# Kernel optimization log

Hardware: AMD Instinct MI355X
Metric: run time of the kernel (lower is better)

The kernel has to match this reference:

```python
import jax, jax.numpy as jnp
import numpy as np

AREA = 4
NUM_HEADS = 4


def _conv1x1(x, w, s, t):
    # 1x1 Conv (bias=False) + folded BatchNorm: per-out-channel scale s, shift t
    y = jnp.einsum('bchw,oc->bohw', x, w)
    return y * s[None, :, None, None] + t[None, :, None, None]


def setup_inputs() -> dict:
    key = jax.random.key(0)
    ks = jax.random.split(key, 9)
    C, heads = 128, NUM_HEADS
    x = jax.random.normal(ks[0], (2, C, 80, 80), jnp.float32)

    def wmat(k, o, i):
        return jax.random.normal(k, (o, i), jnp.float32) * (i ** -0.5)

    def bn(k, n):
        k1, k2 = jax.random.split(k)
        s = 1.0 + 0.05 * jax.random.normal(k1, (n,), jnp.float32)
        t = 0.05 * jax.random.normal(k2, (n,), jnp.float32)
        return s, t

    w_qk = wmat(ks[1], 2 * C, C); s_qk, t_qk = bn(ks[2], 2 * C)
    w_in = wmat(ks[3], C, C); s_in, t_in = bn(ks[4], C)
    w_out = wmat(ks[5], C, C); s_out, t_out = bn(ks[6], C)
    w_fg = jax.random.normal(ks[7], (heads, heads, 1, 5), jnp.float32) * ((5 * heads) ** -0.5)
    s_fg, t_fg = bn(ks[8], heads)
    return dict(x=x, w_qk=w_qk, s_qk=s_qk, t_qk=t_qk, w_in=w_in, s_in=s_in,
                t_in=t_in, w_out=w_out, s_out=s_out, t_out=t_out,
                w_fg=w_fg, s_fg=s_fg, t_fg=t_fg)


def reference(x, w_qk, s_qk, t_qk, w_in, s_in, t_in, w_out, s_out, t_out, w_fg, s_fg, t_fg):
    B, C, H, W = x.shape
    N = H * W
    heads = NUM_HEADS
    hd = C // heads
    inp = x
    # qk projection -> [B, N, 2C]
    qk = _conv1x1(x, w_qk, s_qk, t_qk).reshape(B, 2 * C, N).transpose(0, 2, 1)
    # input-gated values -> [B, N, C]
    v = jax.nn.sigmoid(_conv1x1(x, w_in, s_in, t_in)) * x
    v = v.reshape(B, C, N).transpose(0, 2, 1)
    # area split
    Be, Na = B * AREA, N // AREA
    qk = qk.reshape(Be, Na, 2 * C)
    v = v.reshape(Be, Na, C)
    q, k = qk[..., :C], qk[..., C:]
    q = q.transpose(0, 2, 1).reshape(Be, heads, hd, Na)
    k = k.transpose(0, 2, 1).reshape(Be, heads, hd, Na)
    v = v.transpose(0, 2, 1).reshape(Be, heads, hd, Na)
    # full NxN attention per area/head
    attn = jnp.einsum('bhdn,bhdm->bhnm', q, k) * (hd ** -0.5)
    attn = jax.nn.softmax(attn, axis=-1)
    # forget gate: (1,5) conv mixing heads along last axis, pad (0,2), BN fold, SiLU
    attn = jax.lax.conv_general_dilated(attn, w_fg, (1, 1), ((0, 0), (2, 2)),
                                        dimension_numbers=('NCHW', 'OIHW', 'NCHW'))
    attn = attn * s_fg[None, :, None, None] + t_fg[None, :, None, None]
    attn = jax.nn.silu(attn)
    # v @ attn^T -> [Be, heads, hd, Na]
    o = jnp.einsum('bhdj,bhij->bhdi', v, attn)
    # merge areas back: [Be,Na,h,hd] -> [B,N,C] -> [B,C,H,W]
    o = o.transpose(0, 3, 1, 2).reshape(B, N, C)
    o = o.reshape(B, H, W, C).transpose(0, 3, 1, 2)
    return jax.nn.sigmoid(_conv1x1(o, w_out, s_out, t_out)) * o + inp
```

## Files before the change

kernel.cpp:

```cpp
#include <hip/hip_runtime.h>
#include <hip/hip_bf16.h>
#include <cstdint>

#define CC 128
#define NN 6400
#define NAa 1600
#define HEADS 4
#define HD 32
#define NB 32
#define MT 64

#define P_ROW 68
#define P_HEAD 1096
#define A_ROW 76
#define A_HEAD 1224
#define PW (HEADS * P_HEAD)
#define AW (HEADS * A_HEAD)
#define HB_IDX(par, qs, hh, lo) (((((par)*2 + (qs))*4 + (hh))*16 + (lo)) * 4)
#define XROW 136

typedef __attribute__((ext_vector_type(8))) short bfrag8;
typedef __attribute__((ext_vector_type(4))) float ffrag4;
typedef union { uint2 u2[2]; bfrag8 f8; } cvt16;

#define LOG2E 1.4426950408889634f
#define QSCL (0.17677669529663687f * 1.4426950408889634f)

__device__ __forceinline__ float sigmoid_fast(float y) {
  return __builtin_amdgcn_rcpf(1.0f + __builtin_amdgcn_exp2f(-LOG2E * y));
}
__device__ __forceinline__ unsigned short f2bf(float f) {
  unsigned u = __float_as_uint(f);
  return (unsigned short)((u + 0x7FFFu + ((u >> 16) & 1u)) >> 16);
}
__device__ __forceinline__ unsigned pk2(float a, float b) {
  float2 f2; f2.x = a; f2.y = b;
  __hip_bfloat162 h = __float22bfloat162_rn(f2);
  union { __hip_bfloat162 h2; unsigned u; } cv; cv.h2 = h;
  return cv.u;
}
__device__ __forceinline__ float bfl(unsigned u) { return __uint_as_float(u << 16); }
__device__ __forceinline__ float bfh(unsigned u) { return __uint_as_float(u & 0xFFFF0000u); }

__global__ __launch_bounds__(256) void prep_kernel(
    const float* __restrict__ w_qk, const float* __restrict__ s_qk,
    const float* __restrict__ w_in, const float* __restrict__ s_in,
    const float* __restrict__ w_out, const float* __restrict__ s_out,
    unsigned short* __restrict__ wqkb, unsigned short* __restrict__ wob) {
  const int blk = blockIdx.x, tid = threadIdx.x;
  if (blk < 8) {
    const int r0 = blk * 48;
    for (int i = tid; i < 6144; i += 256) {
      int r = r0 + (i >> 7), c = i & 127;
      float wv, sv;
      if (r < 2 * CC) { wv = w_qk[r * CC + c]; sv = s_qk[r] * (r < CC ? QSCL : 1.0f); }
      else           { wv = w_in[(r - 2 * CC) * CC + c]; sv = s_in[r - 2 * CC]; }
      wqkb[r * CC + c] = f2bf(wv * sv);
    }
  } else {
    const int r0 = (blk - 8) * 64;
    for (int i = tid; i < 8192; i += 256) {
      int r = r0 + (i >> 7), c = i & 127;
      wob[r * CC + c] = f2bf(w_out[r * CC + c] * s_out[r]);
    }
  }
}

__global__ __launch_bounds__(256) void qkv_kernel(
    const float* __restrict__ x, const unsigned short* __restrict__ wqkb,
    const float* __restrict__ t_qk, const float* __restrict__ t_in,
    unsigned short* __restrict__ qt, unsigned short* __restrict__ kt,
    unsigned short* __restrict__ vb) {
  __shared__ __align__(16) unsigned short xb[16 * XROW];
  const int tid = threadIdx.x;
  const int w = tid >> 6, lane = tid & 63, lo = lane & 15, g = lane >> 4;
  const int blk = blockIdx.x;
  const int b = blk / 400, pt = blk - b * 400;
  const int ng0 = pt * 16;
  const int a = ng0 / NAa, na0 = ng0 - a * NAa;
  const int be = b * 4 + a;
  {
    const int c = tid >> 1, half = tid & 1;
    const float* xr = &x[((size_t)(b * CC + c)) * NN + ng0 + 8 * half];
    const float4 f0 = *(const float4*)xr;
    const float4 f1 = *(const float4*)(xr + 4);
    unsigned short* dst = &xb[(8 * half) * XROW + c];
    dst[0 * XROW] = f2bf(f0.x); dst[1 * XROW] = f2bf(f0.y);
    dst[2 * XROW] = f2bf(f0.z); dst[3 * XROW] = f2bf(f0.w);
    dst[4 * XROW] = f2bf(f1.x); dst[5 * XROW] = f2bf(f1.y);
    dst[6 * XROW] = f2bf(f1.z); dst[7 * XROW] = f2bf(f1.w);
  }
  __syncthreads();
  bfrag8 bf[4];
#pragma unroll
  for (int kk = 0; kk < 4; kk++) bf[kk] = *(const bfrag8*)&xb[lo * XROW + kk * 32 + g * 8];
#pragma unroll
  for (int mt6 = 0; mt6 < 6; mt6++) {
    const int rowbase = (w * 6 + mt6) * 16;
    ffrag4 d = {0.f, 0.f, 0.f, 0.f};
#pragma unroll
    for (int kk = 0; kk < 4; kk++) {
      bfrag8 af = *(const bfrag8*)&wqkb[(size_t)(rowbase + lo) * CC + kk * 32 + g * 8];
      d = __builtin_amdgcn_mfma_f32_16x16x32_bf16(af, bf[kk], d, 0, 0, 0);
    }
    const int r0c = rowbase + 4 * g;
    if (r0c < CC) {
      const int h = r0c >> 5, d0 = r0c & 31;
      uint2 pk;
      pk.x = pk2(d[0] + t_qk[r0c] * QSCL, d[1] + t_qk[r0c + 1] * QSCL);
      pk.y = pk2(d[2] + t_qk[r0c + 2] * QSCL, d[3] + t_qk[r0c + 3] * QSCL);
      *(uint2*)&qt[((size_t)(be * HEADS + h) * NAa + na0 + lo) * HD + d0] = pk;
    } else if (r0c < 2 * CC) {
      const int ch = r0c - CC, h = ch >> 5, d0 = ch & 31;
      uint2 pk;
      pk.x = pk2(d[0] + t_qk[r0c], d[1] + t_qk[r0c + 1]);
      pk.y = pk2(d[2] + t_qk[r0c + 2], d[3] + t_qk[r0c + 3]);
      *(uint2*)&kt[((size_t)(be * HEADS + h) * NAa + na0 + lo) * HD + d0] = pk;
    } else {
      const int ch0 = r0c - 2 * CC;
      const uint2 xv = *(const uint2*)&xb[lo * XROW + ch0];
      float xr[4] = {bfl(xv.x), bfh(xv.x), bfl(xv.y), bfh(xv.y)};
#pragma unroll
      for (int r = 0; r < 4; r++) {
        float y = d[r] + t_in[ch0 + r];
        vb[((size_t)be * CC + ch0 + r) * NAa + na0 + lo] = f2bf(sigmoid_fast(y) * xr[r]);
      }
    }
  }
}

__global__ __launch_bounds__(256) void stats_kernel(
    const unsigned short* __restrict__ qt, const unsigned short* __restrict__ kt,
    float* __restrict__ pstats) {
  int tid = threadIdx.x;
  int h = tid >> 6, lane = tid & 63, lo = lane & 15, g = lane >> 4;
  int bid = blockIdx.x;
  int be = bid & 7;
  int rest = bid >> 3;
  int n0 = (rest % 50) * 32;
  int split = rest / 50;
  int ts0 = split ? 12 : 0, ts1 = split ? 25 : 12;

  const unsigned short* qtb = qt + (size_t)(be * HEADS + h) * NAa * HD;
  const unsigned short* ktb = kt + (size_t)(be * HEADS + h) * NAa * HD;

  bfrag8 qf0 = *(const bfrag8*)(qtb + (size_t)(n0 + lo) * HD + g * 8);
  bfrag8 qf1 = *(const bfrag8*)(qtb + (size_t)(n0 + 16 + lo) * HD + g * 8);
  float sm0[4] = {0.f, 0.f, 0.f, 0.f};
  float sm1[4] = {0.f, 0.f, 0.f, 0.f};
  for (int t = ts0; t < ts1; t++) {
    int m0 = t * MT;
#pragma unroll
    for (int sb = 0; sb < 4; sb++) {
      bfrag8 kf = *(const bfrag8*)(ktb + (size_t)(m0 + sb * 16 + lo) * HD + g * 8);
      ffrag4 z = {0.f, 0.f, 0.f, 0.f};
      ffrag4 c0 = __builtin_amdgcn_mfma_f32_16x16x32_bf16(qf0, kf, z, 0, 0, 0);
      ffrag4 c1 = __builtin_amdgcn_mfma_f32_16x16x32_bf16(qf1, kf, z, 0, 0, 0);
#pragma unroll
      for (int r = 0; r < 4; r++) {
        sm0[r] += __builtin_amdgcn_exp2f(c0[r]);
        sm1[r] += __builtin_amdgcn_exp2f(c1[r]);
      }
    }
  }
#pragma unroll
  for (int r = 0; r < 4; r++) {
#pragma unroll
    for (int off = 1; off <= 8; off <<= 1) {
      sm0[r] += __shfl_xor(sm0[r], off);
      sm1[r] += __shfl_xor(sm1[r], off);
    }
  }
  if (lo == 0) {
    float4 s4; s4.x = sm0[0]; s4.y = sm0[1]; s4.z = sm0[2]; s4.w = sm0[3];
    *(float4*)&pstats[((size_t)(split * 8 + be) * HEADS + h) * NAa + n0 + 4 * g] = s4;
    float4 s5; s5.x = sm1[0]; s5.y = sm1[1]; s5.z = sm1[2]; s5.w = sm1[3];
    *(float4*)&pstats[((size_t)(split * 8 + be) * HEADS + h) * NAa + n0 + 16 + 4 * g] = s5;
  }
}

__global__ __launch_bounds__(512) void apply_kernel(
    const unsigned short* __restrict__ qt, const unsigned short* __restrict__ kt,
    const unsigned short* __restrict__ vb, const float* __restrict__ pstats,
    const float* __restrict__ w_fg, const float* __restrict__ s_fg,
    const float* __restrict__ t_fg, unsigned short* __restrict__ o_part) {
  __shared__ __align__(16) unsigned short Ps[2 * PW];
  __shared__ __align__(16) unsigned short A2s[2 * AW];
  __shared__ __align__(16) unsigned short Hb[1024];
  const int tid = threadIdx.x;
  const int w = tid >> 6, lane = tid & 63, lo = lane & 15, g = lane >> 4;
  const int h = w >> 1, u = w & 1;
  const int bid = blockIdx.x;
  const int be = bid & 7;
  const int rest = bid >> 3;
  const int n0 = (rest % 50) * NB;
  const int split = rest / 50;
  const int ts0 = (split == 0) ? 0 : (split == 1 ? 9 : 17);
  const int tend = (split == 0) ? 9 : (split == 1 ? 17 : 26);
  const int p0 = ts0 & 1;

  const unsigned short* qtb = qt + (size_t)(be * HEADS + h) * NAa * HD;
  const unsigned short* ktb = kt + (size_t)(be * HEADS + h) * NAa * HD;
  const unsigned short* vhb = vb + (size_t)(be * CC + h * HD) * NAa;

  bfrag8 qf[2];
#pragma unroll
  for (int qs = 0; qs < 2; ++qs)
    qf[qs] = *(const bfrag8*)(qtb + (size_t)(n0 + 16 * qs + lo) * HD + g * 8);

  bfrag8 wfrag;
  {
    const int ho = lo >> 2, s = lo & 3;
#pragma unroll
    for (int j = 0; j < 8; j++) {
      const int tp = j - s;
      float wv = (tp >= 0 && tp < 5) ? w_fg[(ho * HEADS + g) * 5 + tp] : 0.0f;
      wfrag[j] = (short)f2bf(wv);
    }
  }
  const float sfv = s_fg[g], tfv = t_fg[g];

  float linv[2];
#pragma unroll
  for (int qs = 0; qs < 2; ++qs) {
    const float den = pstats[((size_t)(0 + be) * HEADS + h) * NAa + n0 + 16 * qs + lo] +
                      pstats[((size_t)(8 + be) * HEADS + h) * NAa + n0 + 16 * qs + lo];
    linv[qs] = -__log2f(den);
  }

  ffrag4 oacc[2][2];
#pragma unroll
  for (int qs = 0; qs < 2; ++qs) {
    ffrag4 z = {0.f, 0.f, 0.f, 0.f};
    oacc[qs][0] = z; oacc[qs][1] = z;
  }

  if (split == 0) {
    if (u == 0 && g == 0) {
      uint2 zz; zz.x = 0; zz.y = 0;
#pragma unroll
      for (int qs = 0; qs < 2; ++qs)
        *(uint2*)&Hb[HB_IDX(p0, qs, h, lo)] = zz;
    }
  } else if (u == 0) {
    bfrag8 kf = *(const bfrag8*)(ktb + (size_t)(ts0 * MT - 16 + lo) * HD + g * 8);
#pragma unroll
    for (int qs = 0; qs < 2; ++qs) {
      ffrag4 cin = {linv[qs], linv[qs], linv[qs], linv[qs]};
      ffrag4 c = __builtin_amdgcn_mfma_f32_16x16x32_bf16(kf, qf[qs], cin, 0, 0, 0);
      if (g == 3) {
        uint2 pk;
        pk.x = pk2(__builtin_amdgcn_exp2f(c[0]), __builtin_amdgcn_exp2f(c[1]));
        pk.y = pk2(__builtin_amdgcn_exp2f(c[2]), __builtin_amdgcn_exp2f(c[3]));
        *(uint2*)&Hb[HB_IDX(p0, qs, h, lo)] = pk;
      }
    }
  }
  {
    const int m0 = ts0 * MT;
#pragma unroll
    for (int sbi = 0; sbi < 2; sbi++) {
      const int sb = 2 * u + sbi;
      bfrag8 kf = *(const bfrag8*)(ktb + (size_t)(m0 + sb * 16 + lo) * HD + g * 8);
#pragma unroll
      for (int qs = 0; qs < 2; ++qs) {
        ffrag4 cin = {linv[qs], linv[qs], linv[qs], linv[qs]};
        ffrag4 c = __builtin_amdgcn_mfma_f32_16x16x32_bf16(kf, qf[qs], cin, 0, 0, 0);
        uint2 pk;
        pk.x = pk2(__builtin_amdgcn_exp2f(c[0]), __builtin_amdgcn_exp2f(c[1]));
        pk.y = pk2(__builtin_amdgcn_exp2f(c[2]), __builtin_amdgcn_exp2f(c[3]));
        *(uint2*)&Ps[qs * PW + h * P_HEAD + lo * P_ROW + 16 * sb + 4 * g] = pk;
        if (sb == 3 && g == 3)
          *(uint2*)&Hb[HB_IDX(p0 ^ 1, qs, h, lo)] = pk;
      }
    }
  }
  __syncthreads();

  for (int t = ts0; t < tend; t++) {
    const int m0 = t * MT;
    const int par = t & 1;
    const bfrag8 vf0 = *(const bfrag8*)(vhb + (size_t)lo * NAa + (m0 - 2 + 32 * u + 8 * g));
    const bfrag8 vf1 = *(const bfrag8*)(vhb + (size_t)(16 + lo) * NAa + (m0 - 2 + 32 * u + 8 * g));
    const bool doqk = (t + 1 < tend);
    const bool realqk = doqk && (t + 1 < 25);
    bfrag8 kf0, kf1;
    if (realqk) {
      const int m1 = (t + 1) * MT;
      kf0 = *(const bfrag8*)(ktb + (size_t)(m1 + (2 * u) * 16 + lo) * HD + g * 8);
      kf1 = *(const bfrag8*)(ktb + (size_t)(m1 + (2 * u + 1) * 16 + lo) * HD + g * 8);
    }
    const bool edge = (t == 0) || (t == 25);
#pragma unroll
    for (int qs = 0; qs < 2; ++qs) {
#pragma unroll
      for (int ii = 0; ii < 2; ii++) {
        const int i = 2 * w + ii;
        cvt16 bb;
        if (i == 0)
          bb.u2[0] = *(const uint2*)&Hb[HB_IDX(par, qs, g, lo)];
        else
          bb.u2[0] = *(const uint2*)&Ps[qs * PW + g * P_HEAD + lo * P_ROW + 4 * i - 4];
        bb.u2[1] = *(const uint2*)&Ps[qs * PW + g * P_HEAD + lo * P_ROW + 4 * i];
        ffrag4 z = {0.f, 0.f, 0.f, 0.f};
        ffrag4 d = __builtin_amdgcn_mfma_f32_16x16x32_bf16(wfrag, bb.f8, z, 0, 0, 0);
        float a2v[4];
        if (edge) {
#pragma unroll
          for (int r = 0; r < 4; r++) {
            const int mp = m0 - 2 + 4 * i + r;
            float y = d[r] * sfv + tfv;
            float v = y * sigmoid_fast(y);
            a2v[r] = (mp >= 0 && mp < NAa) ? v : 0.0f;
          }
        } else {
#pragma unroll
          for (int r = 0; r < 4; r++) {
            float y = d[r] * sfv + tfv;
            a2v[r] = y * sigmoid_fast(y);
          }
        }
        uint2 pk;
        pk.x = pk2(a2v[0], a2v[1]);
        pk.y = pk2(a2v[2], a2v[3]);
        *(uint2*)&A2s[qs * AW + g * A_HEAD + lo * A_ROW + 4 * i] = pk;
      }
    }
    __syncthreads();
    if (doqk) {
      if (realqk) {
#pragma unroll
        for (int qs = 0; qs < 2; ++qs) {
          ffrag4 cin = {linv[qs], linv[qs], linv[qs], linv[qs]};
          ffrag4 c0 = __builtin_amdgcn_mfma_f32_16x16x32_bf16(kf0, qf[qs], cin, 0, 0, 0);
          ffrag4 c1 = __builtin_amdgcn_mfma_f32_16x16x32_bf16(kf1, qf[qs], cin, 0, 0, 0);
          uint2 pk;
          pk.x = pk2(__builtin_amdgcn_exp2f(c0[0]), __builtin_amdgcn_exp2f(c0[1]));
          pk.y = pk2(__builtin_amdgcn_exp2f(c0[2]), __builtin_amdgcn_exp2f(c0[3]));
          *(uint2*)&Ps[qs * PW + h * P_HEAD + lo * P_ROW + 16 * (2 * u) + 4 * g] = pk;
          uint2 pk1;
          pk1.x = pk2(__builtin_amdgcn_exp2f(c1[0]), __builtin_amdgcn_exp2f(c1[1]));
          pk1.y = pk2(__builtin_amdgcn_exp2f(c1[2]), __builtin_amdgcn_exp2f(c1[3]));
          *(uint2*)&Ps[qs * PW + h * P_HEAD + lo * P_ROW + 16 * (2 * u + 1) + 4 * g] = pk1;
          if (u == 1 && g == 3)
            *(uint2*)&Hb[HB_IDX(par, qs, h, lo)] = pk1;
        }
      } else {
        uint2 zz; zz.x = 0; zz.y = 0;
#pragma unroll
        for (int qs = 0; qs < 2; ++qs) {
          *(uint2*)&Ps[qs * PW + h * P_HEAD + lo * P_ROW + 16 * (2 * u) + 4 * g] = zz;
          *(uint2*)&Ps[qs * PW + h * P_HEAD + lo * P_ROW + 16 * (2 * u + 1) + 4 * g] = zz;
        }
      }
    }
#pragma unroll
    for (int qs = 0; qs < 2; ++qs) {
      cvt16 av;
      av.u2[0] = *(const uint2*)&A2s[qs * AW + h * A_HEAD + lo * A_ROW + 32 * u + 8 * g];
      av.u2[1] = *(const uint2*)&A2s[qs * AW + h * A_HEAD + lo * A_ROW + 32 * u + 8 * g + 4];
      oacc[qs][0] = __builtin_amdgcn_mfma_f32_16x16x32_bf16(av.f8, vf0, oacc[qs][0], 0, 0, 0);
      oacc[qs][1] = __builtin_amdgcn_mfma_f32_16x16x32_bf16(av.f8, vf1, oacc[qs][1], 0, 0, 0);
    }
    __syncthreads();
  }

  float* scr = (float*)A2s;
  if (u == 1) {
#pragma unroll
    for (int qs = 0; qs < 2; ++qs) {
      float4 f0; f0.x = oacc[qs][0][0]; f0.y = oacc[qs][0][1]; f0.z = oacc[qs][0][2]; f0.w = oacc[qs][0][3];
      float4 f1; f1.x = oacc[qs][1][0]; f1.y = oacc[qs][1][1]; f1.z = oacc[qs][1][2]; f1.w = oacc[qs][1][3];
      *(float4*)&scr[((qs * 4 + h) * 64 + lane) * 8] = f0;
      *(float4*)&scr[((qs * 4 + h) * 64 + lane) * 8 + 4] = f1;
    }
  }
  __syncthreads();
  if (u == 0) {
#pragma unroll
    for (int qs = 0; qs < 2; ++qs) {
      const float4 f0 = *(const float4*)&scr[((qs * 4 + h) * 64 + lane) * 8];
      const float4 f1 = *(const float4*)&scr[((qs * 4 + h) * 64 + lane) * 8 + 4];
      const float fa[4] = {f0.x, f0.y, f0.z, f0.w};
      const float fb[4] = {f1.x, f1.y, f1.z, f1.w};
#pragma unroll
      for (int r = 0; r < 4; r++) {
        const size_t rowoff = ((size_t)(split * 8 + be) * NAa + n0 + 16 * qs + 4 * g + r) * CC;
        o_part[rowoff + h * HD + lo] = f2bf(oacc[qs][0][r] + fa[r]);
        o_part[rowoff + h * HD + 16 + lo] = f2bf(oacc[qs][1][r] + fb[r]);
      }
    }
  }
}

__global__ __launch_bounds__(256) void out_kernel(
    const unsigned short* __restrict__ o_part, const unsigned short* __restrict__ wob,
    const float* __restrict__ t_out, const float* __restrict__ x,
    float* __restrict__ out) {
  const int tid = threadIdx.x;
  const int w = tid >> 6, lane = tid & 63, lo = lane & 15, g = lane >> 4;
  const int blk = blockIdx.x;
  const int b = blk / 400, pt = blk - b * 400;
  const int ng0 = pt * 16;
  const int a = ng0 / NAa, na0 = ng0 - a * NAa;
  const int be = b * 4 + a;
  const size_t orow0 = ((size_t)(0 * 8 + be) * NAa + na0 + lo) * CC;
  const size_t orow1 = ((size_t)(1 * 8 + be) * NAa + na0 + lo) * CC;
  const size_t orow2 = ((size_t)(2 * 8 + be) * NAa + na0 + lo) * CC;
  bfrag8 bf0[4], bf1[4], bf2[4];
#pragma unroll
  for (int kk = 0; kk < 4; kk++) {
    bf0[kk] = *(const bfrag8*)&o_part[orow0 + kk * 32 + g * 8];
    bf1[kk] = *(const bfrag8*)&o_part[orow1 + kk * 32 + g * 8];
    bf2[kk] = *(const bfrag8*)&o_part[orow2 + kk * 32 + g * 8];
  }
#pragma unroll
  for (int mt2 = 0; mt2 < 2; mt2++) {
    const int rowbase = (w * 2 + mt2) * 16;
    ffrag4 d = {0.f, 0.f, 0.f, 0.f};
#pragma unroll
    for (int kk = 0; kk < 4; kk++) {
      bfrag8 af = *(const bfrag8*)&wob[(size_t)(rowbase + lo) * CC + kk * 32 + g * 8];
      d = __builtin_amdgcn_mfma_f32_16x16x32_bf16(af, bf0[kk], d, 0, 0, 0);
      d = __builtin_amdgcn_mfma_f32_16x16x32_bf16(af, bf1[kk], d, 0, 0, 0);
      d = __builtin_amdgcn_mfma_f32_16x16x32_bf16(af, bf2[kk], d, 0, 0, 0);
    }
    const int ch0 = rowbase + 4 * g;
    const uint2 q0 = *(const uint2*)&o_part[orow0 + ch0];
    const uint2 q1 = *(const uint2*)&o_part[orow1 + ch0];
    const uint2 q2 = *(const uint2*)&o_part[orow2 + ch0];
    float ov[4] = {bfl(q0.x) + bfl(q1.x) + bfl(q2.x), bfh(q0.x) + bfh(q1.x) + bfh(q2.x),
                   bfl(q0.y) + bfl(q1.y) + bfl(q2.y), bfh(q0.y) + bfh(q1.y) + bfh(q2.y)};
#pragma unroll
    for (int r = 0; r < 4; r++) {
      const size_t xi = ((size_t)b * CC + ch0 + r) * NN + ng0 + lo;
      float y = d[r] + t_out[ch0 + r];
      out[xi] = ov[r] * sigmoid_fast(y) + x[xi];
    }
  }
}

extern "C" void kernel_launch(void* const* d_in, const int* in_sizes, int n_in,
                              void* d_out, int out_size, void* d_ws, size_t ws_size,
                              hipStream_t stream) {
  const float* x    = (const float*)d_in[0];
  const float* w_qk = (const float*)d_in[1];
  const float* s_qk = (const float*)d_in[2];
  const float* t_qk = (const float*)d_in[3];
  const float* w_in = (const float*)d_in[4];
  const float* s_in = (const float*)d_in[5];
  const float* t_in = (const float*)d_in[6];
  const float* w_out = (const float*)d_in[7];
  const float* s_out = (const float*)d_in[8];
  const float* t_out = (const float*)d_in[9];
  const float* w_fg = (const float*)d_in[10];
  const float* s_fg = (const float*)d_in[11];
  const float* t_fg = (const float*)d_in[12];

  char* wsb = (char*)d_ws;
  unsigned short* o_part = (unsigned short*)wsb;
  unsigned short* vb_raw = (unsigned short*)(wsb + 9830400);
  unsigned short* vbp = vb_raw + 2;
  unsigned short* qt = (unsigned short*)(wsb + 13107264);
  unsigned short* kt = (unsigned short*)(wsb + 16384064);
  unsigned short* wqkb = (unsigned short*)(wsb + 19660864);
  unsigned short* wob = (unsigned short*)(wsb + 19759168);
  float* pstats = (float*)(wsb + 19791936);
  float* out = (float*)d_out;

  prep_kernel<<<10, 256, 0, stream>>>(w_qk, s_qk, w_in, s_in, w_out, s_out, wqkb, wob);
  qkv_kernel<<<800, 256, 0, stream>>>(x, wqkb, t_qk, t_in, qt, kt, vbp);
  stats_kernel<<<800, 256, 0, stream>>>(qt, kt, pstats);
  apply_kernel<<<1200, 512, 0, stream>>>(qt, kt, vbp, pstats, w_fg, s_fg, t_fg, o_part);
  out_kernel<<<800, 256, 0, stream>>>(o_part, wob, t_out, x, out);
}
```

Before: 122.2 us.

## Shrink apply_kernel blocks to 16 query rows with 256 threads and 2400 blocks

Restructures apply_kernel so each block handles 16 query rows instead of 32. It uses 4 waves (one per head) instead of 8, and each wave now covers the full 64-key tile. This halves shared memory per block and removes the cross-wave reduction of partial outputs through LDS and its extra barrier. Grid size doubles to 2400 blocks for more occupancy, but every block must reload K and V tiles for fewer query rows, which doubles global and L2 traffic for those operands.

```diff
diff --git a/kernel.cpp b/kernel.cpp
--- a/kernel.cpp
+++ b/kernel.cpp
@@ -7,7 +7,6 @@
 #define NAa 1600
 #define HEADS 4
 #define HD 32
-#define NB 32
 #define MT 64
 
 #define P_ROW 68
@@ -16,7 +15,7 @@
 #define A_HEAD 1224
 #define PW (HEADS * P_HEAD)
 #define AW (HEADS * A_HEAD)
-#define HB_IDX(par, qs, hh, lo) (((((par)*2 + (qs))*4 + (hh))*16 + (lo)) * 4)
+#define HB_IDX(par, hh, lo) ((((par)*4 + (hh))*16 + (lo)) * 4)
 #define XROW 136
 
 typedef __attribute__((ext_vector_type(8))) short bfrag8;
@@ -179,22 +178,21 @@
   }
 }
 
-__global__ __launch_bounds__(512) void apply_kernel(
+__global__ __launch_bounds__(256) void apply_kernel(
     const unsigned short* __restrict__ qt, const unsigned short* __restrict__ kt,
     const unsigned short* __restrict__ vb, const float* __restrict__ pstats,
     const float* __restrict__ w_fg, const float* __restrict__ s_fg,
     const float* __restrict__ t_fg, unsigned short* __restrict__ o_part) {
-  __shared__ __align__(16) unsigned short Ps[2 * PW];
-  __shared__ __align__(16) unsigned short A2s[2 * AW];
-  __shared__ __align__(16) unsigned short Hb[1024];
+  __shared__ __align__(16) unsigned short Ps[PW];
+  __shared__ __align__(16) unsigned short A2s[AW];
+  __shared__ __align__(16) unsigned short Hb[512];
   const int tid = threadIdx.x;
-  const int w = tid >> 6, lane = tid & 63, lo = lane & 15, g = lane >> 4;
-  const int h = w >> 1, u = w & 1;
+  const int h = tid >> 6, lane = tid & 63, lo = lane & 15, g = lane >> 4;
   const int bid = blockIdx.x;
   const int be = bid & 7;
   const int rest = bid >> 3;
-  const int n0 = (rest % 50) * NB;
-  const int split = rest / 50;
+  const int n0 = (rest % 100) * 16;
+  const int split = rest / 100;
   const int ts0 = (split == 0) ? 0 : (split == 1 ? 9 : 17);
   const int tend = (split == 0) ? 9 : (split == 1 ? 17 : 26);
   const int p0 = ts0 & 1;
@@ -203,10 +201,7 @@
   const unsigned short* ktb = kt + (size_t)(be * HEADS + h) * NAa * HD;
   const unsigned short* vhb = vb + (size_t)(be * CC + h * HD) * NAa;
 
-  bfrag8 qf[2];
-#pragma unroll
-  for (int qs = 0; qs < 2; ++qs)
-    qf[qs] = *(const bfrag8*)(qtb + (size_t)(n0 + 16 * qs + lo) * HD + g * 8);
+  const bfrag8 qf = *(const bfrag8*)(qtb + (size_t)(n0 + lo) * HD + g * 8);
 
   bfrag8 wfrag;
   {
@@ -220,59 +215,41 @@
   }
   const float sfv = s_fg[g], tfv = t_fg[g];
 
-  float linv[2];
-#pragma unroll
-  for (int qs = 0; qs < 2; ++qs) {
-    const float den = pstats[((size_t)(0 + be) * HEADS + h) * NAa + n0 + 16 * qs + lo] +
-                      pstats[((size_t)(8 + be) * HEADS + h) * NAa + n0 + 16 * qs + lo];
-    linv[qs] = -__log2f(den);
-  }
-
-  ffrag4 oacc[2][2];
-#pragma unroll
-  for (int qs = 0; qs < 2; ++qs) {
-    ffrag4 z = {0.f, 0.f, 0.f, 0.f};
-    oacc[qs][0] = z; oacc[qs][1] = z;
-  }
+  const float den = pstats[((size_t)(0 + be) * HEADS + h) * NAa + n0 + lo] +
+                    pstats[((size_t)(8 + be) * HEADS + h) * NAa + n0 + lo];
+  const float linv = -__log2f(den);
+  const ffrag4 cin = {linv, linv, linv, linv};
+
+  ffrag4 oacc0 = {0.f, 0.f, 0.f, 0.f};
+  ffrag4 oacc1 = {0.f, 0.f, 0.f, 0.f};
 
   if (split == 0) {
-    if (u == 0 && g == 0) {
+    if (g == 0) {
       uint2 zz; zz.x = 0; zz.y = 0;
-#pragma unroll
-      for (int qs = 0; qs < 2; ++qs)
-        *(uint2*)&Hb[HB_IDX(p0, qs, h, lo)] = zz;
-    }
-  } else if (u == 0) {
+      *(uint2*)&Hb[HB_IDX(p0, h, lo)] = zz;
+    }
+  } else {
     bfrag8 kf = *(const bfrag8*)(ktb + (size_t)(ts0 * MT - 16 + lo) * HD + g * 8);
-#pragma unroll
-    for (int qs = 0; qs < 2; ++qs) {
-      ffrag4 cin = {linv[qs], linv[qs], linv[qs], linv[qs]};
-      ffrag4 c = __builtin_amdgcn_mfma_f32_16x16x32_bf16(kf, qf[qs], cin, 0, 0, 0);
-      if (g == 3) {
-        uint2 pk;
-        pk.x = pk2(__builtin_amdgcn_exp2f(c[0]), __builtin_amdgcn_exp2f(c[1]));
-        pk.y = pk2(__builtin_amdgcn_exp2f(c[2]), __builtin_amdgcn_exp2f(c[3]));
-        *(uint2*)&Hb[HB_IDX(p0, qs, h, lo)] = pk;
-      }
+    ffrag4 c = __builtin_amdgcn_mfma_f32_16x16x32_bf16(kf, qf, cin, 0, 0, 0);
+    if (g == 3) {
+      uint2 pk;
+      pk.x = pk2(__builtin_amdgcn_exp2f(c[0]), __builtin_amdgcn_exp2f(c[1]));
+      pk.y = pk2(__builtin_amdgcn_exp2f(c[2]), __builtin_amdgcn_exp2f(c[3]));
+      *(uint2*)&Hb[HB_IDX(p0, h, lo)] = pk;
     }
   }
   {
     const int m0 = ts0 * MT;
 #pragma unroll
-    for (int sbi = 0; sbi < 2; sbi++) {
-      const int sb = 2 * u + sbi;
+    for (int sb = 0; sb < 4; sb++) {
       bfrag8 kf = *(const bfrag8*)(ktb + (size_t)(m0 + sb * 16 + lo) * HD + g * 8);
-#pragma unroll
-      for (int qs = 0; qs < 2; ++qs) {
-        ffrag4 cin = {linv[qs], linv[qs], linv[qs], linv[qs]};
-        ffrag4 c = __builtin_amdgcn_mfma_f32_16x16x32_bf16(kf, qf[qs], cin, 0, 0, 0);
-        uint2 pk;
-        pk.x = pk2(__builtin_amdgcn_exp2f(c[0]), __builtin_amdgcn_exp2f(c[1]));
-        pk.y = pk2(__builtin_amdgcn_exp2f(c[2]), __builtin_amdgcn_exp2f(c[3]));
-        *(uint2*)&Ps[qs * PW + h * P_HEAD + lo * P_ROW + 16 * sb + 4 * g] = pk;
-        if (sb == 3 && g == 3)
-          *(uint2*)&Hb[HB_IDX(p0 ^ 1, qs, h, lo)] = pk;
-      }
+      ffrag4 c = __builtin_amdgcn_mfma_f32_16x16x32_bf16(kf, qf, cin, 0, 0, 0);
+      uint2 pk;
+      pk.x = pk2(__builtin_amdgcn_exp2f(c[0]), __builtin_amdgcn_exp2f(c[1]));
+      pk.y = pk2(__builtin_amdgcn_exp2f(c[2]), __builtin_amdgcn_exp2f(c[3]));
+      *(uint2*)&Ps[h * P_HEAD + lo * P_ROW + 16 * sb + 4 * g] = pk;
+      if (sb == 3 && g == 3)
+        *(uint2*)&Hb[HB_IDX(p0 ^ 1, h, lo)] = pk;
     }
   }
   __syncthreads();
@@ -280,116 +257,90 @@
   for (int t = ts0; t < tend; t++) {
     const int m0 = t * MT;
     const int par = t & 1;
-    const bfrag8 vf0 = *(const bfrag8*)(vhb + (size_t)lo * NAa + (m0 - 2 + 32 * u + 8 * g));
-    const bfrag8 vf1 = *(const bfrag8*)(vhb + (size_t)(16 + lo) * NAa + (m0 - 2 + 32 * u + 8 * g));
+    bfrag8 vf[2][2];
+#pragma unroll
+    for (int u = 0; u < 2; ++u) {
+      vf[u][0] = *(const bfrag8*)(vhb + (size_t)lo * NAa + (m0 - 2 + 32 * u + 8 * g));
+      vf[u][1] = *(const bfrag8*)(vhb + (size_t)(16 + lo) * NAa + (m0 - 2 + 32 * u + 8 * g));
+    }
     const bool doqk = (t + 1 < tend);
     const bool realqk = doqk && (t + 1 < 25);
-    bfrag8 kf0, kf1;
+    bfrag8 kfp[4];
     if (realqk) {
       const int m1 = (t + 1) * MT;
-      kf0 = *(const bfrag8*)(ktb + (size_t)(m1 + (2 * u) * 16 + lo) * HD + g * 8);
-      kf1 = *(const bfrag8*)(ktb + (size_t)(m1 + (2 * u + 1) * 16 + lo) * HD + g * 8);
+#pragma unroll
+      for (int sb = 0; sb < 4; sb++)
+        kfp[sb] = *(const bfrag8*)(ktb + (size_t)(m1 + sb * 16 + lo) * HD + g * 8);
     }
     const bool edge = (t == 0) || (t == 25);
 #pragma unroll
-    for (int qs = 0; qs < 2; ++qs) {
-#pragma unroll
-      for (int ii = 0; ii < 2; ii++) {
-        const int i = 2 * w + ii;
-        cvt16 bb;
-        if (i == 0)
-          bb.u2[0] = *(const uint2*)&Hb[HB_IDX(par, qs, g, lo)];
-        else
-          bb.u2[0] = *(const uint2*)&Ps[qs * PW + g * P_HEAD + lo * P_ROW + 4 * i - 4];
-        bb.u2[1] = *(const uint2*)&Ps[qs * PW + g * P_HEAD + lo * P_ROW + 4 * i];
-        ffrag4 z = {0.f, 0.f, 0.f, 0.f};
-        ffrag4 d = __builtin_amdgcn_mfma_f32_16x16x32_bf16(wfrag, bb.f8, z, 0, 0, 0);
-        float a2v[4];
-        if (edge) {
-#pragma unroll
-          for (int r = 0; r < 4; r++) {
-            const int mp = m0 - 2 + 4 * i + r;
-            float y = d[r] * sfv + tfv;
-            float v = y * sigmoid_fast(y);
-            a2v[r] = (mp >= 0 && mp < NAa) ? v : 0.0f;
-          }
-        } else {
-#pragma unroll
-          for (int r = 0; r < 4; r++) {
-            float y = d[r] * sfv + tfv;
-            a2v[r] = y * sigmoid_fast(y);
-          }
+    for (int ii = 0; ii < 4; ii++) {
+      const int i = 4 * h + ii;
+      cvt16 bb;
+      if (i == 0)
+        bb.u2[0] = *(const uint2*)&Hb[HB_IDX(par, g, lo)];
+      else
+        bb.u2[0] = *(const uint2*)&Ps[g * P_HEAD + lo * P_ROW + 4 * i - 4];
+      bb.u2[1] = *(const uint2*)&Ps[g * P_HEAD + lo * P_ROW + 4 * i];
+      ffrag4 z = {0.f, 0.f, 0.f, 0.f};
+      ffrag4 d = __builtin_amdgcn_mfma_f32_16x16x32_bf16(wfrag, bb.f8, z, 0, 0, 0);
+      float a2v[4];
+      if (edge) {
+#pragma unroll
+        for (int r = 0; r < 4; r++) {
+          const int mp = m0 - 2 + 4 * i + r;
+          float y = d[r] * sfv + tfv;
+          float v = y * sigmoid_fast(y);
+          a2v[r] = (mp >= 0 && mp < NAa) ? v : 0.0f;
         }
-        uint2 pk;
-        pk.x = pk2(a2v[0], a2v[1]);
-        pk.y = pk2(a2v[2], a2v[3]);
-        *(uint2*)&A2s[qs * AW + g * A_HEAD + lo * A_ROW + 4 * i] = pk;
+      } else {
+#pragma unroll
+        for (int r = 0; r < 4; r++) {
+          float y = d[r] * sfv + tfv;
+          a2v[r] = y * sigmoid_fast(y);
+        }
       }
+      uint2 pk;
+      pk.x = pk2(a2v[0], a2v[1]);
+      pk.y = pk2(a2v[2], a2v[3]);
+      *(uint2*)&A2s[g * A_HEAD + lo * A_ROW + 4 * i] = pk;
     }
     __syncthreads();
     if (doqk) {
       if (realqk) {
 #pragma unroll
-        for (int qs = 0; qs < 2; ++qs) {
-          ffrag4 cin = {linv[qs], linv[qs], linv[qs], linv[qs]};
-          ffrag4 c0 = __builtin_amdgcn_mfma_f32_16x16x32_bf16(kf0, qf[qs], cin, 0, 0, 0);
-          ffrag4 c1 = __builtin_amdgcn_mfma_f32_16x16x32_bf16(kf1, qf[qs], cin, 0, 0, 0);
+        for (int sb = 0; sb < 4; sb++) {
+          ffrag4 c = __builtin_amdgcn_mfma_f32_16x16x32_bf16(kfp[sb], qf, cin, 0, 0, 0);
           uint2 pk;
-          pk.x = pk2(__builtin_amdgcn_exp2f(c0[0]), __builtin_amdgcn_exp2f(c0[1]));
-          pk.y = pk2(__builtin_amdgcn_exp2f(c0[2]), __builtin_amdgcn_exp2f(c0[3]));
-          *(uint2*)&Ps[qs * PW + h * P_HEAD + lo * P_ROW + 16 * (2 * u) + 4 * g] = pk;
-          uint2 pk1;
-          pk1.x = pk2(__builtin_amdgcn_exp2f(c1[0]), __builtin_amdgcn_exp2f(c1[1]));
-          pk1.y = pk2(__builtin_amdgcn_exp2f(c1[2]), __builtin_amdgcn_exp2f(c1[3]));
-          *(uint2*)&Ps[qs * PW + h * P_HEAD + lo * P_ROW + 16 * (2 * u + 1) + 4 * g] = pk1;
-          if (u == 1 && g == 3)
-            *(uint2*)&Hb[HB_IDX(par, qs, h, lo)] = pk1;
+          pk.x = pk2(__builtin_amdgcn_exp2f(c[0]), __builtin_amdgcn_exp2f(c[1]));
+          pk.y = pk2(__builtin_amdgcn_exp2f(c[2]), __builtin_amdgcn_exp2f(c[3]));
+          *(uint2*)&Ps[h * P_HEAD + lo * P_ROW + 16 * sb + 4 * g] = pk;
+          if (sb == 3 && g == 3)
+            *(uint2*)&Hb[HB_IDX(par, h, lo)] = pk;
         }
       } else {
         uint2 zz; zz.x = 0; zz.y = 0;
 #pragma unroll
-        for (int qs = 0; qs < 2; ++qs) {
-          *(uint2*)&Ps[qs * PW + h * P_HEAD + lo * P_ROW + 16 * (2 * u) + 4 * g] = zz;
-          *(uint2*)&Ps[qs * PW + h * P_HEAD + lo * P_ROW + 16 * (2 * u + 1) + 4 * g] = zz;
-        }
+        for (int sb = 0; sb < 4; sb++)
+          *(uint2*)&Ps[h * P_HEAD + lo * P_ROW + 16 * sb + 4 * g] = zz;
       }
     }
 #pragma unroll
-    for (int qs = 0; qs < 2; ++qs) {
+    for (int u = 0; u < 2; ++u) {
       cvt16 av;
-      av.u2[0] = *(const uint2*)&A2s[qs * AW + h * A_HEAD + lo * A_ROW + 32 * u + 8 * g];
-      av.u2[1] = *(const uint2*)&A2s[qs * AW + h * A_HEAD + lo * A_ROW + 32 * u + 8 * g + 4];
-      oacc[qs][0] = __builtin_amdgcn_mfma_f32_16x16x32_bf16(av.f8, vf0, oacc[qs][0], 0, 0, 0);
-      oacc[qs][1] = __builtin_amdgcn_mfma_f32_16x16x32_bf16(av.f8, vf1, oacc[qs][1], 0, 0, 0);
+      av.u2[0] = *(const uint2*)&A2s[h * A_HEAD + lo * A_ROW + 32 * u + 8 * g];
+      av.u2[1] = *(const uint2*)&A2s[h * A_HEAD + lo * A_ROW + 32 * u + 8 * g + 4];
+      oacc0 = __builtin_amdgcn_mfma_f32_16x16x32_bf16(av.f8, vf[u][0], oacc0, 0, 0, 0);
+      oacc1 = __builtin_amdgcn_mfma_f32_16x16x32_bf16(av.f8, vf[u][1], oacc1, 0, 0, 0);
     }
     __syncthreads();
   }
 
-  float* scr = (float*)A2s;
-  if (u == 1) {
-#pragma unroll
-    for (int qs = 0; qs < 2; ++qs) {
-      float4 f0; f0.x = oacc[qs][0][0]; f0.y = oacc[qs][0][1]; f0.z = oacc[qs][0][2]; f0.w = oacc[qs][0][3];
-      float4 f1; f1.x = oacc[qs][1][0]; f1.y = oacc[qs][1][1]; f1.z = oacc[qs][1][2]; f1.w = oacc[qs][1][3];
-      *(float4*)&scr[((qs * 4 + h) * 64 + lane) * 8] = f0;
-      *(float4*)&scr[((qs * 4 + h) * 64 + lane) * 8 + 4] = f1;
-    }
-  }
-  __syncthreads();
-  if (u == 0) {
-#pragma unroll
-    for (int qs = 0; qs < 2; ++qs) {
-      const float4 f0 = *(const float4*)&scr[((qs * 4 + h) * 64 + lane) * 8];
-      const float4 f1 = *(const float4*)&scr[((qs * 4 + h) * 64 + lane) * 8 + 4];
-      const float fa[4] = {f0.x, f0.y, f0.z, f0.w};
-      const float fb[4] = {f1.x, f1.y, f1.z, f1.w};
-#pragma unroll
-      for (int r = 0; r < 4; r++) {
-        const size_t rowoff = ((size_t)(split * 8 + be) * NAa + n0 + 16 * qs + 4 * g + r) * CC;
-        o_part[rowoff + h * HD + lo] = f2bf(oacc[qs][0][r] + fa[r]);
-        o_part[rowoff + h * HD + 16 + lo] = f2bf(oacc[qs][1][r] + fb[r]);
-      }
-    }
+#pragma unroll
+  for (int r = 0; r < 4; r++) {
+    const size_t rowoff = ((size_t)(split * 8 + be) * NAa + n0 + 4 * g + r) * CC;
+    o_part[rowoff + h * HD + lo] = f2bf(oacc0[r]);
+    o_part[rowoff + h * HD + 16 + lo] = f2bf(oacc1[r]);
   }
 }
 
@@ -471,6 +422,6 @@
   prep_kernel<<<10, 256, 0, stream>>>(w_qk, s_qk, w_in, s_in, w_out, s_out, wqkb, wob);
   qkv_kernel<<<800, 256, 0, stream>>>(x, wqkb, t_qk, t_in, qt, kt, vbp);
   stats_kernel<<<800, 256, 0, stream>>>(qt, kt, pstats);
-  apply_kernel<<<1200, 512, 0, stream>>>(qt, kt, vbp, pstats, w_fg, s_fg, t_fg, o_part);
+  apply_kernel<<<2400, 256, 0, stream>>>(qt, kt, vbp, pstats, w_fg, s_fg, t_fg, o_part);
   out_kernel<<<800, 256, 0, stream>>>(o_part, wob, t_out, x, out);
 }
```

Result: slower. 133.4 us (+9.1%).
